# Kernel optimization log

Measured on AMD Instinct MI355X. Metric: run time of the kernel, lower is better.

Reference implementation:

```python
import jax, jax.numpy as jnp
import numpy as np

B, T, NG, NP = 128, 100, 4096, 512


def setup_inputs() -> dict:
    key = jax.random.key(0)
    ks = jax.random.split(key, 6)
    return {
        "v": jax.random.normal(ks[0], (B, T, 2), dtype=jnp.float32) * 0.1,
        "p0": jax.random.normal(ks[1], (B, NP), dtype=jnp.float32),
        # Linear(Np->Ng, bias=False): weight [Ng, Np]
        "W_enc": jax.random.normal(ks[2], (NG, NP), dtype=jnp.float32) / np.sqrt(NP),
        # nn.RNN weights: W_ih [Ng, 2], W_hh [Ng, Ng], bias=False
        "W_ih": jax.random.normal(ks[3], (NG, 2), dtype=jnp.float32) / np.sqrt(2.0),
        "W_hh": jax.random.normal(ks[4], (NG, NG), dtype=jnp.float32) / np.sqrt(NG),
        # Linear(Ng->Np, bias=True): weight [Np, Ng], bias [Np]
        "W_dec": jax.random.normal(ks[5], (NP, NG), dtype=jnp.float32) / np.sqrt(NG),
        "b_dec": jnp.zeros((NP,), dtype=jnp.float32),
    }


def reference(v, p0, W_enc, W_ih, W_hh, W_dec, b_dec):
    # init hidden state: encoder(p0)  -> [B, Ng]
    h0 = p0 @ W_enc.T
    # precompute input projection for all steps: [T, B, Ng]
    vin = jnp.einsum('bti,gi->tbg', v, W_ih)

    def step(h, x_t):
        h_new = jnp.tanh(x_t + h @ W_hh.T)  # Elman tanh cell, bias=False
        return h_new, h_new

    _, g = jax.lax.scan(step, h0, vin)      # g: [T, B, Ng]
    g = jnp.swapaxes(g, 0, 1)               # [B, T, Ng]
    # decoder: place cell predictions [B, T, Np]
    place_preds = g @ W_dec.T + b_dec
    return place_preds
```

## Files before the change

### kernel.cpp

```cpp
#include <hip/hip_runtime.h>
#include <stdint.h>

namespace {
constexpr int kT = 100;
constexpr int kNG = 4096;
constexpr int kNP = 512;

__device__ __forceinline__ uint16_t f2bf(float f) {
  uint32_t u = __float_as_uint(f);
  u += 0x7FFFu + ((u >> 16) & 1u);
  return (uint16_t)(u >> 16);
}

__device__ __forceinline__ float fast_tanh(float x) {
  float xc = fminf(fmaxf(x, -15.f), 15.f);
  float e = __expf(2.f * xc);
  return (e - 1.f) / (e + 1.f);
}

__device__ __forceinline__ void gl2lds16(const void* g, void* l) {
  __builtin_amdgcn_global_load_lds((const __attribute__((address_space(1))) unsigned int*)g,
                                   (__attribute__((address_space(3))) unsigned int*)l, 16, 0, 0);
}

__device__ __forceinline__ size_t a_img_off(int b, int g) {
  return ((size_t)(((g >> 7) * 8 + (b >> 4)) * 4 + ((g >> 5) & 3)) * 64 +
          ((g >> 3) & 3) * 16 + (b & 15)) * 8 + (g & 7);
}
}

typedef short bf16x8 __attribute__((ext_vector_type(8)));
typedef float f32x4 __attribute__((ext_vector_type(4)));

__global__ __launch_bounds__(512) void cvt_whh_kernel(const float* __restrict__ W,
                                                      uint16_t* __restrict__ WhS,
                                                      int* __restrict__ flags) {
  if (blockIdx.x == 4095) {
    for (int i = threadIdx.x; i < 2048; i += 512) flags[i] = 0;
  }
  const int idx = blockIdx.x * 512 + threadIdx.x;
  const int g = idx >> 9;
  const int k0 = (idx & 511) << 3;
  const float4 x = *(const float4*)(W + (size_t)g * kNG + k0);
  const float4 y = *(const float4*)(W + (size_t)g * kNG + k0 + 4);
  uint4 u;
  u.x = (uint32_t)f2bf(x.x) | ((uint32_t)f2bf(x.y) << 16);
  u.y = (uint32_t)f2bf(x.z) | ((uint32_t)f2bf(x.w) << 16);
  u.z = (uint32_t)f2bf(y.x) | ((uint32_t)f2bf(y.y) << 16);
  u.w = (uint32_t)f2bf(y.z) | ((uint32_t)f2bf(y.w) << 16);
  const int gt = g >> 7, c = g & 127;
  const int nt = c >> 4, col = c & 15;
  const int chunk = k0 >> 7, ktl = (k0 >> 5) & 3, half = (k0 >> 3) & 3;
  const size_t off = ((size_t)(((gt * 32 + chunk) * 8 + nt) * 4 + ktl) * 64 + half * 16 + col) * 8;
  *(uint4*)(WhS + off) = u;
}

__global__ __launch_bounds__(512) void cvt_wdec_kernel(const float* __restrict__ W,
                                                       uint16_t* __restrict__ WdS) {
  const int idx = blockIdx.x * 512 + threadIdx.x;
  const int p = idx >> 9;
  const int k0 = (idx & 511) << 3;
  const float4 x = *(const float4*)(W + (size_t)p * kNG + k0);
  const float4 y = *(const float4*)(W + (size_t)p * kNG + k0 + 4);
  uint4 u;
  u.x = (uint32_t)f2bf(x.x) | ((uint32_t)f2bf(x.y) << 16);
  u.y = (uint32_t)f2bf(x.z) | ((uint32_t)f2bf(x.w) << 16);
  u.z = (uint32_t)f2bf(y.x) | ((uint32_t)f2bf(y.y) << 16);
  u.w = (uint32_t)f2bf(y.z) | ((uint32_t)f2bf(y.w) << 16);
  const int pt = p >> 7, c = p & 127;
  const int nt = c >> 4, col = c & 15;
  const int chunk = k0 >> 7, ktl = (k0 >> 5) & 3, half = (k0 >> 3) & 3;
  const size_t off = ((size_t)(((pt * 32 + chunk) * 8 + nt) * 4 + ktl) * 64 + half * 16 + col) * 8;
  *(uint4*)(WdS + off) = u;
}

__global__ __launch_bounds__(512, 2) void enc_kernel(const float* __restrict__ p0,
                                                     const float* __restrict__ Wenc,
                                                     uint16_t* __restrict__ H0S) {
  __shared__ alignas(16) uint16_t Wlds[16 * 64 * 8];
  const int tid = threadIdx.x;
  const int g0 = blockIdx.x * 16;
  for (int f = tid; f < 16 * 64; f += 512) {
    const int kt = f >> 6, fl = f & 63;
    const int g = g0 + (fl & 15);
    const int k = kt * 32 + ((fl >> 4) << 3);
    const float* s = Wenc + (size_t)g * kNP + k;
    uint16_t* d = Wlds + f * 8;
#pragma unroll
    for (int j = 0; j < 8; j++) d[j] = f2bf(s[j]);
  }
  __syncthreads();
  const int wave = tid >> 6;
  const int lane = tid & 63;
  const int mrow = wave * 16 + (lane & 15);
  const float* arow = p0 + (size_t)mrow * kNP + ((lane >> 4) << 3);
  f32x4 acc = {0.f, 0.f, 0.f, 0.f};
#pragma unroll
  for (int kt = 0; kt < 16; kt++) {
    const float* ap = arow + kt * 32;
    bf16x8 a;
#pragma unroll
    for (int j = 0; j < 8; j++) a[j] = (short)f2bf(ap[j]);
    bf16x8 b = *(const bf16x8*)(Wlds + (kt * 64 + lane) * 8);
    acc = __builtin_amdgcn_mfma_f32_16x16x32_bf16(a, b, acc, 0, 0, 0);
  }
  const int gcol = g0 + (lane & 15);
  const int rbase = wave * 16 + ((lane >> 4) << 2);
#pragma unroll
  for (int r = 0; r < 4; r++) {
    H0S[a_img_off(rbase + r, gcol)] = f2bf(acc[r]);
  }
}

__global__ __launch_bounds__(512, 2) void rnn_loop_kernel(const uint16_t* __restrict__ WhS,
                                                          const uint16_t* __restrict__ H0S,
                                                          uint16_t* __restrict__ Gsw,
                                                          float* __restrict__ Part,
                                                          const float* __restrict__ v,
                                                          const float* __restrict__ Wih,
                                                          int* __restrict__ flags) {
  extern __shared__ uint16_t wlds[];
  const int tid = threadIdx.x;
  const int wave = tid >> 6, lane = tid & 63;
  const int bid = blockIdx.x;
  const int xcd = bid & 7;
  const int gt = xcd * 4 + (bid >> 6);
  const int ks = (bid >> 3) & 7;
  const int mg = wave >> 1, ng = wave & 1;

  int* pcnt = flags;
  int* hcnt = flags + 32 * 32;

  {
    const uint16_t* src = WhS + ((size_t)gt << 19) + ((size_t)(ks * 4) << 14);
#pragma unroll
    for (int i = 0; i < 16; i++) {
      const int j = wave * 16 + i;
      gl2lds16(src + (j << 9) + (lane << 3), (void*)(wlds + (j << 9)));
    }
  }
  __syncthreads();

  const int rbred = ks * 16 + (tid >> 5);
  const int gl = (tid & 31) << 2;
  const int gg = gt * 128 + gl;
  float* myPart = Part + (((size_t)(gt * 8 + ks)) << 14);

  const float4 w0 = *(const float4*)(Wih + gg * 2);
  const float4 w1 = *(const float4*)(Wih + gg * 2 + 4);

  for (int t = 0; t < kT; t++) {
    if (t > 0) {
      const int target = 8 * t;
      if (tid < 5) {
        int* f = (tid < 4) ? (hcnt + ((ks * 4 + tid) << 5)) : (hcnt + (gt << 5));
        while (__hip_atomic_load(f, __ATOMIC_RELAXED, __HIP_MEMORY_SCOPE_AGENT) < target)
          __builtin_amdgcn_s_sleep(1);
      }
      __builtin_amdgcn_fence(__ATOMIC_ACQUIRE, "workgroup");
      __syncthreads();
    }

    const float v0 = v[(rbred * kT + t) * 2 + 0];
    const float v1 = v[(rbred * kT + t) * 2 + 1];

    const uint16_t* Aimg = (t == 0) ? H0S : (Gsw + (((size_t)(t - 1)) << 19));
    f32x4 acc[2][4];
#pragma unroll
    for (int i = 0; i < 2; i++)
#pragma unroll
      for (int j = 0; j < 4; j++) acc[i][j] = (f32x4){0.f, 0.f, 0.f, 0.f};

#pragma unroll
    for (int kc = 0; kc < 4; kc++) {
      const uint16_t* Ac = Aimg + ((size_t)(ks * 4 + kc) << 14);
      bf16x8 a[2][4];
#pragma unroll
      for (int mi = 0; mi < 2; mi++)
#pragma unroll
        for (int ktl = 0; ktl < 4; ktl++)
          a[mi][ktl] = *(const bf16x8*)(Ac + ((((mg * 2 + mi) * 4 + ktl) * 64 + lane) << 3));
#pragma unroll
      for (int ktl = 0; ktl < 4; ktl++) {
#pragma unroll
        for (int nt = 0; nt < 4; nt++) {
          bf16x8 b = *(const bf16x8*)(wlds + (kc << 14) +
                                      ((((ng * 4 + nt) * 4 + ktl) * 64 + lane) << 3));
          acc[0][nt] = __builtin_amdgcn_mfma_f32_16x16x32_bf16(a[0][ktl], b, acc[0][nt], 0, 0, 0);
          acc[1][nt] = __builtin_amdgcn_mfma_f32_16x16x32_bf16(a[1][ktl], b, acc[1][nt], 0, 0, 0);
        }
      }
    }
    {
      const int gcol0 = (ng << 6);
      const int rbase = (mg << 5) + ((lane >> 4) << 2);
#pragma unroll
      for (int mi = 0; mi < 2; mi++)
#pragma unroll
        for (int nt = 0; nt < 4; nt++)
#pragma unroll
          for (int r = 0; r < 4; r++) {
            const int b = rbase + (mi << 4) + r;
            const int g = gcol0 + (nt << 4) + (lane & 15);
            myPart[(b << 7) + g] = acc[mi][nt][r];
          }
    }
    asm volatile("s_waitcnt vmcnt(0)" ::: "memory");
    __syncthreads();
    if (tid == 0) {
      __hip_atomic_fetch_add(pcnt + (gt << 5), 1, __ATOMIC_RELAXED, __HIP_MEMORY_SCOPE_AGENT);
      const int tgt = 8 * (t + 1);
      while (__hip_atomic_load(pcnt + (gt << 5), __ATOMIC_RELAXED, __HIP_MEMORY_SCOPE_AGENT) < tgt)
        __builtin_amdgcn_s_sleep(1);
      __builtin_amdgcn_fence(__ATOMIC_ACQUIRE, "workgroup");
    }
    __syncthreads();

    {
      const float* pb = Part + (((size_t)(gt * 8)) << 14) + (rbred << 7) + gl;
      f32x4 pv[8];
#pragma unroll
      for (int j = 0; j < 8; j++) {
        asm volatile("global_load_dwordx4 %0, %1, off sc0"
                     : "=v"(pv[j])
                     : "v"(pb + ((size_t)j << 14))
                     : "memory");
      }
      asm volatile("s_waitcnt vmcnt(0)" ::: "memory");
      __builtin_amdgcn_sched_barrier(0);
      float s0 = 0.f, s1 = 0.f, s2 = 0.f, s3 = 0.f;
#pragma unroll
      for (int j = 0; j < 8; j++) {
        s0 += pv[j][0]; s1 += pv[j][1]; s2 += pv[j][2]; s3 += pv[j][3];
      }
      const uint16_t h0 = f2bf(fast_tanh(s0 + v0 * w0.x + v1 * w0.y));
      const uint16_t h1 = f2bf(fast_tanh(s1 + v0 * w0.z + v1 * w0.w));
      const uint16_t h2 = f2bf(fast_tanh(s2 + v0 * w1.x + v1 * w1.y));
      const uint16_t h3 = f2bf(fast_tanh(s3 + v0 * w1.z + v1 * w1.w));
      const uint32_t lo = (uint32_t)h0 | ((uint32_t)h1 << 16);
      const uint32_t hi = (uint32_t)h2 | ((uint32_t)h3 << 16);
      const unsigned long long uval = ((unsigned long long)hi << 32) | lo;
      uint16_t* Gt = Gsw + (((size_t)t) << 19);
      __hip_atomic_exchange((unsigned long long*)(Gt + a_img_off(rbred, gg)), uval,
                            __ATOMIC_RELAXED, __HIP_MEMORY_SCOPE_AGENT);
    }
    asm volatile("s_waitcnt vmcnt(0)" ::: "memory");
    __syncthreads();
    if (tid == 0)
      __hip_atomic_fetch_add(hcnt + (gt << 5), 1, __ATOMIC_RELAXED, __HIP_MEMORY_SCOPE_AGENT);
  }
}

__global__ __launch_bounds__(512, 4) void stepmm_kernel(const uint16_t* __restrict__ Asrc,
                                                        const uint16_t* __restrict__ WhS,
                                                        float* __restrict__ Part) {
  __shared__ alignas(16) uint16_t lds[32768];
  const int tid = threadIdx.x;
  const int wave = tid >> 6, lane = tid & 63;
  const int gt = blockIdx.x >> 3, ks = blockIdx.x & 7;
  const int mg = wave >> 1, ng = wave & 1;
  const uint16_t* Wbase = WhS + ((size_t)gt << 19);
  f32x4 acc[2][4];
#pragma unroll
  for (int i = 0; i < 2; i++)
#pragma unroll
    for (int j = 0; j < 4; j++) acc[i][j] = (f32x4){0.f, 0.f, 0.f, 0.f};

  for (int kc = 0; kc < 4; kc++) {
    const int chunk = ks * 4 + kc;
    const uint16_t* Ac = Asrc + ((size_t)chunk << 14);
    const uint16_t* Bc = Wbase + ((size_t)chunk << 14);
#pragma unroll
    for (int i = 0; i < 8; i++) {
      const int j = wave * 8 + i;
      const uint16_t* s = (j < 32) ? (Ac + (j << 9)) : (Bc + ((j - 32) << 9));
      gl2lds16(s + (lane << 3), (void*)(lds + (j << 9)));
    }
    __syncthreads();
    const uint16_t* lA = lds;
    const uint16_t* lB = lds + 16384;
#pragma unroll
    for (int ktl = 0; ktl < 4; ktl++) {
      bf16x8 a0 = *(const bf16x8*)(lA + ((((mg * 2 + 0) * 4 + ktl) * 64 + lane) << 3));
      bf16x8 a1 = *(const bf16x8*)(lA + ((((mg * 2 + 1) * 4 + ktl) * 64 + lane) << 3));
#pragma unroll
      for (int nt = 0; nt < 4; nt++) {
        bf16x8 b = *(const bf16x8*)(lB + ((((ng * 4 + nt) * 4 + ktl) * 64 + lane) << 3));
        acc[0][nt] = __builtin_amdgcn_mfma_f32_16x16x32_bf16(a0, b, acc[0][nt], 0, 0, 0);
        acc[1][nt] = __builtin_amdgcn_mfma_f32_16x16x32_bf16(a1, b, acc[1][nt], 0, 0, 0);
      }
    }
    __syncthreads();
  }
  const int g0 = (gt << 7) + (ng << 6);
  const int rb = (mg << 5) + ((lane >> 4) << 2);
#pragma unroll
  for (int mi = 0; mi < 2; mi++)
#pragma unroll
    for (int nt = 0; nt < 4; nt++)
#pragma unroll
      for (int r = 0; r < 4; r++) {
        const int b = rb + (mi << 4) + r;
        const int g = g0 + (nt << 4) + (lane & 15);
        Part[(((size_t)(ks * 128 + b)) << 12) + g] = acc[mi][nt][r];
      }
}

__global__ __launch_bounds__(256) void steptanh_kernel(const float* __restrict__ Part,
                                                       const float* __restrict__ v,
                                                       const float* __restrict__ Wih,
                                                       uint16_t* __restrict__ Gt, int t) {
  const int tg = blockIdx.x * 256 + threadIdx.x;
  const int b = tg >> 9;
  const int g0 = (tg & 511) << 3;
  float s[8];
#pragma unroll
  for (int j = 0; j < 8; j++) s[j] = 0.f;
#pragma unroll
  for (int ks = 0; ks < 8; ks++) {
    const float4* p = (const float4*)(Part + (((size_t)(ks * 128 + b)) << 12) + g0);
    const float4 x = p[0], y = p[1];
    s[0] += x.x; s[1] += x.y; s[2] += x.z; s[3] += x.w;
    s[4] += y.x; s[5] += y.y; s[6] += y.z; s[7] += y.w;
  }
  const float v0 = v[(b * kT + t) * 2 + 0];
  const float v1 = v[(b * kT + t) * 2 + 1];
  uint16_t h[8];
#pragma unroll
  for (int j = 0; j < 8; j++) {
    const int g = g0 + j;
    const float pre = s[j] + v0 * Wih[g * 2 + 0] + v1 * Wih[g * 2 + 1];
    h[j] = f2bf(fast_tanh(pre));
  }
  uint4 u;
  u.x = (uint32_t)h[0] | ((uint32_t)h[1] << 16);
  u.y = (uint32_t)h[2] | ((uint32_t)h[3] << 16);
  u.z = (uint32_t)h[4] | ((uint32_t)h[5] << 16);
  u.w = (uint32_t)h[6] | ((uint32_t)h[7] << 16);
  const size_t off = ((size_t)(((g0 >> 7) * 8 + (b >> 4)) * 4 + ((g0 >> 5) & 3)) * 64 +
                      ((g0 >> 3) & 3) * 16 + (b & 15)) * 8;
  *(uint4*)(Gt + off) = u;
}

__global__ __launch_bounds__(512, 4) void dec_kernel(const uint16_t* __restrict__ Gsw,
                                                     const uint16_t* __restrict__ WdS,
                                                     const float* __restrict__ bd,
                                                     float* __restrict__ out) {
  __shared__ alignas(16) uint16_t lds[32768];
  const int slot = blockIdx.x & 7;
  const int m = blockIdx.x >> 3;
  const int t = slot + ((m >> 2) << 3);
  const int pt = m & 3;
  if (t >= kT) return;
  const int tid = threadIdx.x;
  const int wave = tid >> 6, lane = tid & 63;
  const int mg = wave >> 1, ng = wave & 1;
  const uint16_t* Abase = Gsw + (size_t)t * 524288;
  const uint16_t* Bbase = WdS + (size_t)pt * 524288;
  f32x4 acc[2][4];
#pragma unroll
  for (int i = 0; i < 2; i++)
#pragma unroll
    for (int j = 0; j < 4; j++) acc[i][j] = (f32x4){0.f, 0.f, 0.f, 0.f};

  for (int chunk = 0; chunk < 32; chunk++) {
    const uint16_t* Ac = Abase + ((size_t)chunk << 14);
    const uint16_t* Bc = Bbase + ((size_t)chunk << 14);
#pragma unroll
    for (int i = 0; i < 8; i++) {
      const int j = wave * 8 + i;
      const uint16_t* s = (j < 32) ? (Ac + (j << 9)) : (Bc + ((j - 32) << 9));
      gl2lds16(s + (lane << 3), (void*)(lds + (j << 9)));
    }
    __syncthreads();
    const uint16_t* lA = lds;
    const uint16_t* lB = lds + 16384;
#pragma unroll
    for (int ktl = 0; ktl < 4; ktl++) {
      bf16x8 a0 = *(const bf16x8*)(lA + ((((mg * 2 + 0) * 4 + ktl) * 64 + lane) << 3));
      bf16x8 a1 = *(const bf16x8*)(lA + ((((mg * 2 + 1) * 4 + ktl) * 64 + lane) << 3));
#pragma unroll
      for (int nt = 0; nt < 4; nt++) {
        bf16x8 b = *(const bf16x8*)(lB + ((((ng * 4 + nt) * 4 + ktl) * 64 + lane) << 3));
        acc[0][nt] = __builtin_amdgcn_mfma_f32_16x16x32_bf16(a0, b, acc[0][nt], 0, 0, 0);
        acc[1][nt] = __builtin_amdgcn_mfma_f32_16x16x32_bf16(a1, b, acc[1][nt], 0, 0, 0);
      }
    }
    __syncthreads();
  }
  const int p0c = (pt << 7) + (ng << 6);
  const int rb = (mg << 5) + ((lane >> 4) << 2);
#pragma unroll
  for (int mi = 0; mi < 2; mi++)
#pragma unroll
    for (int nt = 0; nt < 4; nt++) {
      const int p = p0c + (nt << 4) + (lane & 15);
      const float bias = bd[p];
#pragma unroll
      for (int r = 0; r < 4; r++) {
        const int b = rb + (mi << 4) + r;
        out[((size_t)b * kT + t) * kNP + p] = acc[mi][nt][r] + bias;
      }
    }
}

extern "C" void kernel_launch(void* const* d_in, const int* in_sizes, int n_in,
                              void* d_out, int out_size, void* d_ws, size_t ws_size,
                              hipStream_t stream) {
  const float* v    = (const float*)d_in[0];
  const float* p0   = (const float*)d_in[1];
  const float* Wenc = (const float*)d_in[2];
  const float* Wih  = (const float*)d_in[3];
  const float* Whh  = (const float*)d_in[4];
  const float* Wdec = (const float*)d_in[5];
  const float* bdec = (const float*)d_in[6];
  float* out = (float*)d_out;

  uint8_t* ws = (uint8_t*)d_ws;
  uint16_t* WhS = (uint16_t*)(ws);
  uint16_t* WdS = (uint16_t*)(ws + 33554432);
  uint16_t* H0S = (uint16_t*)(ws + 37748736);
  uint16_t* Gsw = (uint16_t*)(ws + 38797312);
  float*    Part = (float*)(ws + 143654912);
  int*      flags = (int*)(ws + 160432128);

  cvt_whh_kernel<<<4096, 512, 0, stream>>>(Whh, WhS, flags);
  cvt_wdec_kernel<<<512, 512, 0, stream>>>(Wdec, WdS);
  enc_kernel<<<256, 512, 0, stream>>>(p0, Wenc, H0S);

  const uint16_t* WhS_c = WhS;
  const uint16_t* H0S_c = H0S;
  void* args[7] = {(void*)&WhS_c, (void*)&H0S_c, (void*)&Gsw, (void*)&Part,
                   (void*)&v, (void*)&Wih, (void*)&flags};
  hipError_t e = hipLaunchCooperativeKernel(rnn_loop_kernel, dim3(256), dim3(512), args,
                                            (unsigned int)131072, stream);
  if (e != hipSuccess) {
    (void)hipGetLastError();
    for (int t = 0; t < kT; t++) {
      const uint16_t* Asrc = (t == 0) ? H0S : (Gsw + (size_t)(t - 1) * 524288);
      stepmm_kernel<<<256, 512, 0, stream>>>(Asrc, WhS, Part);
      steptanh_kernel<<<256, 256, 0, stream>>>(Part, v, Wih, Gsw + (size_t)t * 524288, t);
    }
  }

  dec_kernel<<<416, 512, 0, stream>>>(Gsw, WdS, bdec, out);
}
```

Baseline: 1.132 ms.

## Store split-K partial sums as bf16 and write weight images coalesced

The RNN loop now writes its per-step split-K partial sums to global memory as bf16 rather than fp32, and the reducing blocks read them back with dwordx2 loads instead of dwordx4. This halves the partial-sum traffic on the serialized per-timestep critical path. The cost is extra rounding of partial sums before the tanh, which can add error. Separately, the weight conversion kernels now index by output position so their stores are contiguous, with the gathers moved to the reads.

```diff
diff --git a/kernel.cpp b/kernel.cpp
--- a/kernel.cpp
+++ b/kernel.cpp
@@ -12,6 +12,10 @@
   return (uint16_t)(u >> 16);
 }
 
+__device__ __forceinline__ float bfbits(uint32_t lo16) {
+  return __uint_as_float(lo16 << 16);
+}
+
 __device__ __forceinline__ float fast_tanh(float x) {
   float xc = fminf(fmaxf(x, -15.f), 15.f);
   float e = __expf(2.f * xc);
@@ -31,6 +35,7 @@
 
 typedef short bf16x8 __attribute__((ext_vector_type(8)));
 typedef float f32x4 __attribute__((ext_vector_type(4)));
+typedef uint32_t u32x2 __attribute__((ext_vector_type(2)));
 
 __global__ __launch_bounds__(512) void cvt_whh_kernel(const float* __restrict__ W,
                                                       uint16_t* __restrict__ WhS,
@@ -38,40 +43,36 @@
   if (blockIdx.x == 4095) {
     for (int i = threadIdx.x; i < 2048; i += 512) flags[i] = 0;
   }
-  const int idx = blockIdx.x * 512 + threadIdx.x;
-  const int g = idx >> 9;
-  const int k0 = (idx & 511) << 3;
+  const int u = blockIdx.x * 512 + threadIdx.x;
+  const int col = u & 15, half = (u >> 4) & 3, ktl = (u >> 6) & 3;
+  const int nt = (u >> 8) & 7, chunk = (u >> 11) & 31, gt = u >> 16;
+  const int g = gt * 128 + nt * 16 + col;
+  const int k0 = chunk * 128 + ktl * 32 + half * 8;
   const float4 x = *(const float4*)(W + (size_t)g * kNG + k0);
   const float4 y = *(const float4*)(W + (size_t)g * kNG + k0 + 4);
-  uint4 u;
-  u.x = (uint32_t)f2bf(x.x) | ((uint32_t)f2bf(x.y) << 16);
-  u.y = (uint32_t)f2bf(x.z) | ((uint32_t)f2bf(x.w) << 16);
-  u.z = (uint32_t)f2bf(y.x) | ((uint32_t)f2bf(y.y) << 16);
-  u.w = (uint32_t)f2bf(y.z) | ((uint32_t)f2bf(y.w) << 16);
-  const int gt = g >> 7, c = g & 127;
-  const int nt = c >> 4, col = c & 15;
-  const int chunk = k0 >> 7, ktl = (k0 >> 5) & 3, half = (k0 >> 3) & 3;
-  const size_t off = ((size_t)(((gt * 32 + chunk) * 8 + nt) * 4 + ktl) * 64 + half * 16 + col) * 8;
-  *(uint4*)(WhS + off) = u;
+  uint4 o;
+  o.x = (uint32_t)f2bf(x.x) | ((uint32_t)f2bf(x.y) << 16);
+  o.y = (uint32_t)f2bf(x.z) | ((uint32_t)f2bf(x.w) << 16);
+  o.z = (uint32_t)f2bf(y.x) | ((uint32_t)f2bf(y.y) << 16);
+  o.w = (uint32_t)f2bf(y.z) | ((uint32_t)f2bf(y.w) << 16);
+  *(uint4*)(WhS + (size_t)u * 8) = o;
 }
 
 __global__ __launch_bounds__(512) void cvt_wdec_kernel(const float* __restrict__ W,
                                                        uint16_t* __restrict__ WdS) {
-  const int idx = blockIdx.x * 512 + threadIdx.x;
-  const int p = idx >> 9;
-  const int k0 = (idx & 511) << 3;
+  const int u = blockIdx.x * 512 + threadIdx.x;
+  const int col = u & 15, half = (u >> 4) & 3, ktl = (u >> 6) & 3;
+  const int nt = (u >> 8) & 7, chunk = (u >> 11) & 31, pt = u >> 16;
+  const int p = pt * 128 + nt * 16 + col;
+  const int k0 = chunk * 128 + ktl * 32 + half * 8;
   const float4 x = *(const float4*)(W + (size_t)p * kNG + k0);
   const float4 y = *(const float4*)(W + (size_t)p * kNG + k0 + 4);
-  uint4 u;
-  u.x = (uint32_t)f2bf(x.x) | ((uint32_t)f2bf(x.y) << 16);
-  u.y = (uint32_t)f2bf(x.z) | ((uint32_t)f2bf(x.w) << 16);
-  u.z = (uint32_t)f2bf(y.x) | ((uint32_t)f2bf(y.y) << 16);
-  u.w = (uint32_t)f2bf(y.z) | ((uint32_t)f2bf(y.w) << 16);
-  const int pt = p >> 7, c = p & 127;
-  const int nt = c >> 4, col = c & 15;
-  const int chunk = k0 >> 7, ktl = (k0 >> 5) & 3, half = (k0 >> 3) & 3;
-  const size_t off = ((size_t)(((pt * 32 + chunk) * 8 + nt) * 4 + ktl) * 64 + half * 16 + col) * 8;
-  *(uint4*)(WdS + off) = u;
+  uint4 o;
+  o.x = (uint32_t)f2bf(x.x) | ((uint32_t)f2bf(x.y) << 16);
+  o.y = (uint32_t)f2bf(x.z) | ((uint32_t)f2bf(x.w) << 16);
+  o.z = (uint32_t)f2bf(y.x) | ((uint32_t)f2bf(y.y) << 16);
+  o.w = (uint32_t)f2bf(y.z) | ((uint32_t)f2bf(y.w) << 16);
+  *(uint4*)(WdS + (size_t)u * 8) = o;
 }
 
 __global__ __launch_bounds__(512, 2) void enc_kernel(const float* __restrict__ p0,
@@ -130,6 +131,7 @@
 
   int* pcnt = flags;
   int* hcnt = flags + 32 * 32;
+  uint16_t* PartB = (uint16_t*)Part;
 
   {
     const uint16_t* src = WhS + ((size_t)gt << 19) + ((size_t)(ks * 4) << 14);
@@ -144,7 +146,7 @@
   const int rbred = ks * 16 + (tid >> 5);
   const int gl = (tid & 31) << 2;
   const int gg = gt * 128 + gl;
-  float* myPart = Part + (((size_t)(gt * 8 + ks)) << 14);
+  uint16_t* myPart = PartB + (((size_t)(gt * 8 + ks)) << 14);
 
   const float4 w0 = *(const float4*)(Wih + gg * 2);
   const float4 w1 = *(const float4*)(Wih + gg * 2 + 4);
@@ -202,7 +204,7 @@
           for (int r = 0; r < 4; r++) {
             const int b = rbase + (mi << 4) + r;
             const int g = gcol0 + (nt << 4) + (lane & 15);
-            myPart[(b << 7) + g] = acc[mi][nt][r];
+            myPart[(b << 7) + g] = f2bf(acc[mi][nt][r]);
           }
     }
     asm volatile("s_waitcnt vmcnt(0)" ::: "memory");
@@ -217,11 +219,11 @@
     __syncthreads();
 
     {
-      const float* pb = Part + (((size_t)(gt * 8)) << 14) + (rbred << 7) + gl;
-      f32x4 pv[8];
+      const uint16_t* pb = PartB + (((size_t)(gt * 8)) << 14) + (rbred << 7) + gl;
+      u32x2 pv[8];
 #pragma unroll
       for (int j = 0; j < 8; j++) {
-        asm volatile("global_load_dwordx4 %0, %1, off sc0"
+        asm volatile("global_load_dwordx2 %0, %1, off sc0"
                      : "=v"(pv[j])
                      : "v"(pb + ((size_t)j << 14))
                      : "memory");
@@ -231,7 +233,10 @@
       float s0 = 0.f, s1 = 0.f, s2 = 0.f, s3 = 0.f;
 #pragma unroll
       for (int j = 0; j < 8; j++) {
-        s0 += pv[j][0]; s1 += pv[j][1]; s2 += pv[j][2]; s3 += pv[j][3];
+        s0 += bfbits(pv[j][0] & 0xFFFFu);
+        s1 += __uint_as_float(pv[j][0] & 0xFFFF0000u);
+        s2 += bfbits(pv[j][1] & 0xFFFFu);
+        s3 += __uint_as_float(pv[j][1] & 0xFFFF0000u);
       }
       const uint16_t h0 = f2bf(fast_tanh(s0 + v0 * w0.x + v1 * w0.y));
       const uint16_t h1 = f2bf(fast_tanh(s1 + v0 * w0.z + v1 * w0.w));
```

New measurement: 1.072 ms. -5.3%, faster.
